# Kernel optimization log

Hardware: AMD Instinct MI355X
Metric: run time of the kernel (lower is better)

The kernel has to match this reference:

```python
import jax, jax.numpy as jnp
import numpy as np

EPS = 1e-5
K_NBR = 21   # num_neighbors + 1 (self)
PSI = 4


def _bn(x, g, b):
    # BatchNorm (training-mode forward): channel-last, normalize over all other axes
    axes = tuple(range(x.ndim - 1))
    m = jnp.mean(x, axis=axes, keepdims=True)
    v = jnp.var(x, axis=axes, keepdims=True)
    return (x - m) * jax.lax.rsqrt(v + EPS) * g + b


def setup_inputs() -> dict:
    key = jax.random.key(0)
    ks = jax.random.split(key, 16)
    B, N, Cin, Cout = 4, 2048, 64, 256
    h = Cout // 2
    w_ch = Cout // PSI
    heads = 2 * PSI - 1

    def w(k, o, i):
        return jax.random.normal(k, (o, i), dtype=jnp.float32) * (1.0 / np.sqrt(i))

    p = {}
    p['xyz'] = jax.random.normal(ks[0], (B, N, 3), dtype=jnp.float32)
    p['f'] = jax.random.normal(ks[1], (B, Cin, N), dtype=jnp.float32)
    p['W_geo'] = w(ks[2], h, 6);       p['g_geo'] = jnp.ones(h);   p['b_geo'] = jnp.zeros(h)
    p['W_feat'] = w(ks[3], h, 2 * Cin); p['g_feat'] = jnp.ones(h); p['b_feat'] = jnp.zeros(h)
    p['g_bn'] = jnp.ones(Cout); p['b_bn'] = jnp.zeros(Cout)
    p['W_q'] = w(ks[4], Cout, Cout); p['g_q'] = jnp.ones(Cout); p['b_q'] = jnp.zeros(Cout)
    p['W_k'] = w(ks[5], Cout, Cout); p['g_k'] = jnp.ones(Cout); p['b_k'] = jnp.zeros(Cout)
    p['W_v'] = w(ks[6], Cout, Cout); p['g_v'] = jnp.ones(Cout); p['b_v'] = jnp.zeros(Cout)
    p['W_fus'] = w(ks[7], Cout, heads * w_ch); p['bias_fus'] = jnp.zeros(Cout)
    p['g_fus'] = jnp.ones(Cout); p['b_fus'] = jnp.zeros(Cout)
    p['g_ln'] = jnp.ones(Cout); p['b_ln'] = jnp.zeros(Cout)
    p['W_mlp'] = w(ks[8], Cout, Cout); p['bias_mlp'] = jnp.zeros(Cout)
    return p


def reference(xyz, f, W_geo, g_geo, b_geo, W_feat, g_feat, b_feat, g_bn, b_bn,
              W_q, g_q, b_q, W_k, g_k, b_k, W_v, g_v, b_v,
              W_fus, bias_fus, g_fus, b_fus, g_ln, b_ln, W_mlp, bias_mlp):
    B, N, _ = xyz.shape
    Cout = g_bn.shape[0]
    w_ch = Cout // PSI
    d_sh = w_ch // 2
    heads = 2 * PSI - 1

    # ---- PositionFusion: KNN grouping ----
    sq = jnp.sum(xyz * xyz, axis=-1)                                   # [B,N]
    d2 = sq[:, :, None] + sq[:, None, :] - 2.0 * jnp.einsum('bnd,bmd->bnm', xyz, xyz)
    _, idx = jax.lax.top_k(-d2, K_NBR)                                 # [B,N,K]

    grouped_xyz = jax.vmap(lambda p, i: p[i])(xyz, idx)                # [B,N,K,3]
    xyz_diff = grouped_xyz - xyz[:, :, None, :]
    geo_in = jnp.concatenate(
        [jnp.broadcast_to(xyz[:, :, None, :], grouped_xyz.shape), xyz_diff], axis=-1)  # [B,N,K,6]

    ft = jnp.transpose(f, (0, 2, 1))                                   # [B,N,Cin]
    grouped_f = jax.vmap(lambda p, i: p[i])(ft, idx)                   # [B,N,K,Cin]
    feat_in = jnp.concatenate(
        [grouped_f, jnp.broadcast_to(ft[:, :, None, :], grouped_f.shape)], axis=-1)    # [B,N,K,2Cin]

    geo = jax.nn.relu(_bn(jnp.einsum('bnki,oi->bnko', geo_in, W_geo), g_geo, b_geo))
    fea = jax.nn.relu(_bn(jnp.einsum('bnki,oi->bnko', feat_in, W_feat), g_feat, b_feat))
    feature_ = jnp.max(jnp.concatenate([geo, fea], axis=-1), axis=2)   # [B,N,Cout] (maxpool over K)

    # ---- BatchNorm1d ----
    x = _bn(feature_, g_bn, b_bn)

    # ---- Shifted-channel multi-head attention ----
    q = jax.nn.relu(_bn(jnp.einsum('bnc,oc->bno', x, W_q), g_q, b_q))
    k = jax.nn.relu(_bn(jnp.einsum('bnc,oc->bno', x, W_k), g_k, b_k))
    v = jax.nn.relu(_bn(jnp.einsum('bnc,oc->bno', x, W_v), g_v, b_v))

    qh = jnp.stack([q[..., m * d_sh:m * d_sh + w_ch] for m in range(heads)], axis=1)  # [B,H,N,w]
    kh = jnp.stack([k[..., m * d_sh:m * d_sh + w_ch] for m in range(heads)], axis=1)
    vh = jnp.stack([v[..., m * d_sh:m * d_sh + w_ch] for m in range(heads)], axis=1)

    a = jax.nn.softmax(jnp.einsum('bhnc,bhmc->bhnm', qh, kh), axis=-1)  # [B,H,N,N]
    o = jnp.einsum('bhnm,bhmc->bhnc', a, vh)                            # [B,H,N,w]
    O = jnp.transpose(o, (0, 2, 1, 3)).reshape(B, N, heads * w_ch)      # channel-concat per head

    fus = jax.nn.relu(_bn(jnp.einsum('bnc,oc->bno', O, W_fus) + bias_fus, g_fus, b_fus))

    feature__ = fus + feature_                                          # residual

    # ---- LayerNorm over channels ----
    m = jnp.mean(feature__, axis=-1, keepdims=True)
    var = jnp.var(feature__, axis=-1, keepdims=True)
    y = (feature__ - m) * jax.lax.rsqrt(var + EPS) * g_ln + b_ln

    out = feature__ + (jnp.einsum('bnc,oc->bno', y, W_mlp) + bias_mlp)
    return jnp.transpose(out, (0, 2, 1))                                # [B,Cout,N] like torch
```

## Files before the change

kernel.cpp:

```cpp
#include <hip/hip_runtime.h>
#include <math.h>

#define NB    4
#define NPTS  2048
#define ROWS  (NB*NPTS)
#define CIN   64
#define COUT  256
#define KNBR  21
#define NHEADS 7
#define WCH   64
#define DSH   32

typedef __attribute__((ext_vector_type(8))) short short8;
typedef __attribute__((ext_vector_type(4))) float floatx4;

__device__ __forceinline__ ushort f2bf(float x) {
    unsigned u = __float_as_uint(x);
    u += 0x7fffu + ((u >> 16) & 1u);
    return (ushort)(u >> 16);
}

template<int N>
__device__ __forceinline__ float dpp_ror16(float x) {
    return __int_as_float(__builtin_amdgcn_update_dpp(
        0, __float_as_int(x), 0x120 | N, 0xF, 0xF, true));
}
__device__ __forceinline__ float dpp_max16(float x) {
    x = fmaxf(x, dpp_ror16<1>(x));
    x = fmaxf(x, dpp_ror16<2>(x));
    x = fmaxf(x, dpp_ror16<4>(x));
    x = fmaxf(x, dpp_ror16<8>(x));
    return x;
}
__device__ __forceinline__ float dpp_sum16(float x) {
    x += dpp_ror16<1>(x);
    x += dpp_ror16<2>(x);
    x += dpp_ror16<4>(x);
    x += dpp_ror16<8>(x);
    return x;
}

template<int CTRL, int RMASK>
__device__ __forceinline__ unsigned dpp_umin_step(unsigned x) {
    unsigned t = (unsigned)__builtin_amdgcn_update_dpp((int)x, (int)x, CTRL, RMASK, 0xF, false);
    return (t < x) ? t : x;
}
__device__ __forceinline__ unsigned wave_min_u32(unsigned x) {
    x = dpp_umin_step<0x111, 0xF>(x);
    x = dpp_umin_step<0x112, 0xF>(x);
    x = dpp_umin_step<0x114, 0xF>(x);
    x = dpp_umin_step<0x118, 0xF>(x);
    x = dpp_umin_step<0x142, 0xA>(x);
    x = dpp_umin_step<0x143, 0xC>(x);
    return (unsigned)__builtin_amdgcn_readlane((int)x, 63);
}

__global__ __launch_bounds__(256) void prep_knn(const float* __restrict__ f, const float* __restrict__ Wf,
                                                const float* __restrict__ xyz, const float* __restrict__ Wg,
                                                const float* __restrict__ W_q, const float* __restrict__ W_k,
                                                const float* __restrict__ W_v,
                                                float* __restrict__ X, float* __restrict__ A,
                                                ushort* __restrict__ Wb, float* __restrict__ sums,
                                                int* __restrict__ idx) {
    __shared__ float4 SXQ[2048];
    int t = threadIdx.x;
    int blk = blockIdx.x;
    if (blk < 512) {
        float* As = (float*)SXQ;
        float* Ws = As + 16*68;
        int bx = blk & 127, by = blk >> 7;
        if (by == 0 && bx < 12) sums[bx*256 + t] = 0.f;
        int gid = (by*128 + bx)*256 + t;
        for (int i = gid; i < 196608; i += 131072) {
            const float* Wsrc = (i < 65536) ? W_q : (i < 131072) ? W_k : W_v;
            Wb[i] = f2bf(Wsrc[i & 65535]);
        }
        int r0 = bx * 64, n0 = by * 64;
        for (int e = t; e < 4096; e += 256) {
            int row = r0 + (e >> 6), c = n0 + (e & 63), cc = c & 127;
            float x = xyz[row*3], y = xyz[row*3+1], z = xyz[row*3+2];
            const float* w = Wg + cc*6;
            float s = (c < 128) ? ((w[3]*x + w[4]*y) + w[5]*z)
                                : (((w[0]-w[3])*x + (w[1]-w[4])*y) + (w[2]-w[5])*z);
            A[(size_t)row*256 + c] = s;
        }
        int b = r0 >> 11, nbase = r0 & 2047;
        int tx = t & 15, ty = t >> 4;
        float acc[4][4];
#pragma unroll
        for (int i = 0; i < 4; i++)
#pragma unroll
            for (int j = 0; j < 4; j++) acc[i][j] = 0.f;
        int m64 = t & 63, kg = t >> 6;
        int lk = t & 15, lm = t >> 4;
        for (int k0 = 0; k0 < 64; k0 += 16) {
#pragma unroll
            for (int p = 0; p < 4; p++) {
                int k = kg*4 + p;
                As[k*68 + m64] = f[(size_t)b*CIN*NPTS + (size_t)(k0 + k)*NPTS + nbase + m64];
            }
#pragma unroll
            for (int i2 = 0; i2 < 4; i2++) {
                int cg = n0 + lm + 16*i2;
                Ws[lk*68 + lm + 16*i2] = Wf[(size_t)(cg & 127)*128 + (cg >> 7)*64 + k0 + lk];
            }
            __syncthreads();
#pragma unroll
            for (int kq = 0; kq < 16; kq++) {
                float4 a  = *(const float4*)&As[kq*68 + 4*ty];
                float4 b4 = *(const float4*)&Ws[kq*68 + 4*tx];
                float av[4] = {a.x, a.y, a.z, a.w};
                float bv[4] = {b4.x, b4.y, b4.z, b4.w};
#pragma unroll
                for (int i = 0; i < 4; i++)
#pragma unroll
                    for (int j = 0; j < 4; j++) acc[i][j] = fmaf(av[i], bv[j], acc[i][j]);
            }
            __syncthreads();
        }
#pragma unroll
        for (int i = 0; i < 4; i++)
#pragma unroll
            for (int j = 0; j < 4; j++)
                X[(size_t)(r0 + 4*ty + i)*256 + n0 + 4*tx + j] = acc[i][j];
        return;
    }
    int kb = blk - 512;
    int b = kb >> 9;
    int g = kb & 511;
    for (int m = t; m < NPTS; m += 256) {
        float x = xyz[(size_t)b*NPTS*3 + m*3];
        float y = xyz[(size_t)b*NPTS*3 + m*3 + 1];
        float z = xyz[(size_t)b*NPTS*3 + m*3 + 2];
        SXQ[m] = make_float4(x, y, z, (x*x + y*y) + z*z);
    }
    __syncthreads();
    int w = t >> 6, lane = t & 63;
    int n = g*4 + w;
    float4 q4 = SXQ[n];
    float qx = q4.x, qy = q4.y, qz = q4.z, sqn = q4.w;
    unsigned key[32];
#pragma unroll
    for (int i = 0; i < 32; i++) {
        int m = lane + (i << 6);
        float4 p = SXQ[m];
        float dt = (qx*p.x + qy*p.y) + qz*p.z;
        float d2 = fmaxf((sqn + p.w) - 2.0f*dt, 0.f);
        key[i] = (__float_as_uint(d2) & 0xFFFFF800u) | (unsigned)m;
    }
    unsigned winkey = 0xFFFFFFFFu;
    for (int kk = 0; kk < 32; kk++) {
        unsigned lv = key[0];
#pragma unroll
        for (int i = 1; i < 32; i++) lv = (key[i] < lv) ? key[i] : lv;
        unsigned win = wave_min_u32(lv);
        if (lane == kk) winkey = win;
        unsigned widx = win & 2047u;
        int slot = (int)(widx >> 6);
        bool own = (lane == (int)(widx & 63u));
#pragma unroll
        for (int i = 0; i < 32; i++)
            if (i == slot && own) key[i] = 0xFFFFFFFFu;
    }
    double d2r;
    int mr;
    {
        double qx64 = (double)qx, qy64 = (double)qy, qz64 = (double)qz;
        double sqn64 = qx64*qx64 + qy64*qy64 + qz64*qz64;
        if (lane < 32) {
            mr = (int)(winkey & 2047u);
            float4 p = SXQ[mr];
            double x = (double)p.x, y = (double)p.y, z = (double)p.z;
            double sqm = x*x + y*y + z*z;
            double dt  = qx64*x + qy64*y + qz64*z;
            d2r = (sqn64 + sqm) - 2.0*dt;
        } else {
            d2r = INFINITY; mr = 0x7FFFFFFF;
        }
    }
#pragma unroll
    for (int k = 2; k <= 32; k <<= 1) {
#pragma unroll
        for (int j = k >> 1; j > 0; j >>= 1) {
            double od = __shfl_xor(d2r, j, 64);
            int    om = __shfl_xor(mr, j, 64);
            bool up    = ((lane & k) == 0);
            bool lower = ((lane & j) == 0);
            bool oless = (od < d2r) || (od == d2r && om < mr);
            bool keepOther = up ? (lower ? oless : !oless) : (lower ? !oless : oless);
            if (keepOther) { d2r = od; mr = om; }
        }
    }
    if (lane < KNBR)
        idx[((size_t)b*NPTS + n)*KNBR + lane] = mr;
}

__global__ __launch_bounds__(256) void stats_gf(const float* __restrict__ geoBC, const float* __restrict__ featAC,
                                                const int* __restrict__ idx, const float* __restrict__ g_geo,
                                                const float* __restrict__ g_feat,
                                                float* __restrict__ sums, float* __restrict__ xsel) {
    int c = threadIdx.x;
    int cc = c & 127;
    const float* base = (c < 128) ? geoBC : featAC;
    bool wantmax = ((c < 128) ? g_geo[cc] : g_feat[cc]) >= 0.f;
    float s = 0.f, ss = 0.f;
    int r0 = blockIdx.x * 32;
    for (int r = r0; r < r0 + 32; r++) {
        int b = r >> 11;
        float ctr = base[(size_t)r*256 + 128 + cc];
        float mx = -1e30f, mn = 1e30f;
        const int* ip = idx + (size_t)r*KNBR;
        for (int kk = 0; kk < KNBR; kk++) {
            int j = ip[kk];
            float xv = ctr + base[((size_t)(b*NPTS + j))*256 + cc];
            mx = fmaxf(mx, xv); mn = fminf(mn, xv);
            s += xv; ss += xv*xv;
        }
        xsel[(size_t)r*256 + c] = wantmax ? mx : mn;
    }
    atomicAdd(&sums[c], s);
    atomicAdd(&sums[256 + c], ss);
}

__global__ __launch_bounds__(256) void feature_maxsel(const float* __restrict__ xsel, const float* __restrict__ sums,
                                                      const float* __restrict__ g_geo, const float* __restrict__ b_geo,
                                                      const float* __restrict__ g_feat, const float* __restrict__ b_feat,
                                                      float* __restrict__ feat, float* __restrict__ sums_bn1) {
    int c = threadIdx.x;
    const float inv = 1.0f / (float)(ROWS*KNBR);
    float mean = sums[c]*inv;
    float var  = sums[256+c]*inv - mean*mean;
    float g  = (c < 128) ? g_geo[c] : g_feat[c-128];
    float bb = (c < 128) ? b_geo[c] : b_feat[c-128];
    float sc = g / sqrtf(var + 1e-5f);
    float tt = bb - mean*sc;
    float s = 0.f, ss = 0.f;
    int r0 = blockIdx.x*32;
    for (int r = r0; r < r0+32; r++) {
        size_t i = (size_t)r*256 + c;
        float y = fmaxf(fmaf(sc, xsel[i], tt), 0.f);
        feat[i] = y; s += y; ss += y*y;
    }
    atomicAdd(&sums_bn1[c], s); atomicAdd(&sums_bn1[256+c], ss);
}

__global__ __launch_bounds__(256) void gemm_qkv(const float* __restrict__ Af, const float* __restrict__ sums_in,
                                                const float* __restrict__ g_bn, const float* __restrict__ b_bn,
                                                const ushort* __restrict__ Wb,
                                                float* __restrict__ QKVF, float* __restrict__ sums) {
    __shared__ float bns[2][256];
    __shared__ float red[4][256][2];
    int t = threadIdx.x;
    int r0 = blockIdx.x * 64, g = blockIdx.y;
    int w = t >> 6, lane = t & 63;
    int r15 = lane & 15, quad = lane >> 4;
    {
        float mean = sums_in[512 + t] * (1.0f/(float)ROWS);
        float var  = sums_in[768 + t] * (1.0f/(float)ROWS) - mean*mean;
        float sc = g_bn[t] / sqrtf(var + 1e-5f);
        bns[0][t] = sc;
        bns[1][t] = b_bn[t] - mean*sc;
    }
    __syncthreads();
    short8 aq[8];
    {
        const float* ap = Af + (size_t)(r0 + 16*w + r15)*256;
#pragma unroll
        for (int kc = 0; kc < 8; kc++) {
            int k0 = 32*kc + 8*quad;
            float4 a0 = *(const float4*)&ap[k0];
            float4 a1 = *(const float4*)&ap[k0+4];
            float4 s0 = *(const float4*)&bns[0][k0];
            float4 s1 = *(const float4*)&bns[0][k0+4];
            float4 h0 = *(const float4*)&bns[1][k0];
            float4 h1 = *(const float4*)&bns[1][k0+4];
            ushort u8[8];
            u8[0] = f2bf(fmaf(s0.x, a0.x, h0.x)); u8[1] = f2bf(fmaf(s0.y, a0.y, h0.y));
            u8[2] = f2bf(fmaf(s0.z, a0.z, h0.z)); u8[3] = f2bf(fmaf(s0.w, a0.w, h0.w));
            u8[4] = f2bf(fmaf(s1.x, a1.x, h1.x)); u8[5] = f2bf(fmaf(s1.y, a1.y, h1.y));
            u8[6] = f2bf(fmaf(s1.z, a1.z, h1.z)); u8[7] = f2bf(fmaf(s1.w, a1.w, h1.w));
            aq[kc] = *(short8*)u8;
        }
    }
    floatx4 zero4 = {0.f, 0.f, 0.f, 0.f};
    floatx4 acc[16];
#pragma unroll
    for (int st = 0; st < 16; st++) acc[st] = zero4;
    const ushort* wbase = Wb + (size_t)g*65536 + (size_t)r15*256 + 8*quad;
#pragma unroll
    for (int st = 0; st < 16; st++) {
        const ushort* wp = wbase + (size_t)(16*st)*256;
#pragma unroll
        for (int kc = 0; kc < 8; kc++) {
            short8 bf = *(const short8*)(wp + 32*kc);
            acc[st] = __builtin_amdgcn_mfma_f32_16x16x32_bf16(aq[kc], bf, acc[st], 0, 0, 0);
        }
    }
#pragma unroll
    for (int st = 0; st < 16; st++) {
        float s  = (acc[st][0] + acc[st][1]) + (acc[st][2] + acc[st][3]);
        float q2 = (acc[st][0]*acc[st][0] + acc[st][1]*acc[st][1]) +
                   (acc[st][2]*acc[st][2] + acc[st][3]*acc[st][3]);
        s  += __shfl_xor(s, 16, 64);  s  += __shfl_xor(s, 32, 64);
        q2 += __shfl_xor(q2, 16, 64); q2 += __shfl_xor(q2, 32, 64);
        if (lane < 16) { red[w][16*st + r15][0] = s; red[w][16*st + r15][1] = q2; }
#pragma unroll
        for (int reg = 0; reg < 4; reg++)
            QKVF[(size_t)(r0 + 16*w + 4*quad + reg)*768 + g*256 + 16*st + r15] = acc[st][reg];
    }
    __syncthreads();
    {
        float s = red[0][t][0] + red[1][t][0] + red[2][t][0] + red[3][t][0];
        float q = red[0][t][1] + red[1][t][1] + red[2][t][1] + red[3][t][1];
        atomicAdd(&sums[1024 + g*512 + t], s);
        atomicAdd(&sums[1024 + g*512 + 256 + t], q);
    }
}

__global__ __launch_bounds__(256) void affine_qkv(const float* __restrict__ QKVF, const float* __restrict__ sums,
                                                  const float* __restrict__ g_q, const float* __restrict__ b_q,
                                                  const float* __restrict__ g_k, const float* __restrict__ b_k,
                                                  const float* __restrict__ g_v, const float* __restrict__ b_v,
                                                  ushort* __restrict__ qk, ushort* __restrict__ vt) {
    __shared__ float sts[6][256];
    __shared__ ushort tile[64][72];
    int t = threadIdx.x;
    {
        const float* gs[3] = {g_q, g_k, g_v};
        const float* bs[3] = {b_q, b_k, b_v};
#pragma unroll
        for (int g = 0; g < 3; g++) {
            float mean = sums[1024 + g*512 + t] * (1.0f/(float)ROWS);
            float var  = sums[1024 + g*512 + 256 + t] * (1.0f/(float)ROWS) - mean*mean;
            float sc = gs[g][t] / sqrtf(var + 1e-5f);
            sts[2*g][t] = sc;
            sts[2*g+1][t] = bs[g][t] - mean*sc;
        }
    }
    __syncthreads();
    int r0 = blockIdx.x * 64, c0 = blockIdx.y * 64;
    int b = r0 >> 11, nbase = r0 & 2047;
    if (c0 < 512) {
#pragma unroll
        for (int rep = 0; rep < 16; rep++) {
            int e = t + 256*rep;
            int row = e >> 6, c = e & 63;
            int col = c0 + c, g = col >> 8, cc = col & 255;
            float v = QKVF[(size_t)(r0 + row)*768 + col];
            v = fmaxf(fmaf(sts[2*g][cc], v, sts[2*g+1][cc]), 0.f);
            qk[(size_t)(r0 + row)*512 + col] = f2bf(v);
        }
    } else {
#pragma unroll
        for (int rep = 0; rep < 16; rep++) {
            int e = t + 256*rep;
            int row = e >> 6, c = e & 63;
            int col = c0 + c, cc = col & 255;
            float v = QKVF[(size_t)(r0 + row)*768 + col];
            v = fmaxf(fmaf(sts[4][cc], v, sts[5][cc]), 0.f);
            tile[c][row] = f2bf(v);
        }
        __syncthreads();
#pragma unroll
        for (int rep = 0; rep < 16; rep++) {
            int e = t + 256*rep;
            int cc = e >> 6, nn = e & 63;
            vt[((size_t)(b*256 + (c0 - 512) + cc))*2048 + nbase + nn] = tile[cc][nn];
        }
    }
}

__global__ __launch_bounds__(256) void attn2(const ushort* __restrict__ qk, const ushort* __restrict__ vt,
                                             float* __restrict__ obuf) {
    __shared__ ushort Ksh[64*72];
    __shared__ ushort Vts[64*72];
    __shared__ ushort Psh[128*72];
    int h = blockIdx.y, b = blockIdx.z;
    int r0 = blockIdx.x * 128;
    int t = threadIdx.x;
    int w = t >> 6, lane = t & 63;
    int r15 = lane & 15, quad = lane >> 4;
    size_t rowbase = (size_t)b*NPTS;
    int hoff = h*DSH;

    short8 aq[2][2];
#pragma unroll
    for (int u = 0; u < 2; u++)
#pragma unroll
        for (int s = 0; s < 2; s++)
            aq[u][s] = *(const short8*)(qk + (rowbase + r0 + 64*u + 16*w + r15)*512 + hoff + 32*s + 8*quad);

    floatx4 zero4 = {0.f, 0.f, 0.f, 0.f};
    floatx4 oacc[2][4];
    float mrun[2][4], lrun[2][4];
#pragma unroll
    for (int u = 0; u < 2; u++)
#pragma unroll
        for (int i = 0; i < 4; i++) { oacc[u][i] = zero4; mrun[u][i] = -1e30f; lrun[u][i] = 0.f; }

    for (int m0 = 0; m0 < NPTS; m0 += 64) {
#pragma unroll
        for (int rep = 0; rep < 2; rep++) {
            int e = t + 256*rep;
            int rr = e >> 3, c = e & 7;
            *(uint4*)&Ksh[rr*72 + 8*c] =
                *(const uint4*)(qk + (rowbase + m0 + rr)*512 + 256 + hoff + 8*c);
            *(uint4*)&Vts[rr*72 + 8*c] =
                *(const uint4*)(vt + ((size_t)(b*256 + hoff + rr))*2048 + m0 + 8*c);
        }
        __syncthreads();

        floatx4 sacc[2][4];
#pragma unroll
        for (int u = 0; u < 2; u++)
#pragma unroll
            for (int tt = 0; tt < 4; tt++) sacc[u][tt] = zero4;
#pragma unroll
        for (int tt = 0; tt < 4; tt++) {
            int key = 16*tt + r15;
#pragma unroll
            for (int s = 0; s < 2; s++) {
                short8 kf = *(const short8*)&Ksh[key*72 + 32*s + 8*quad];
#pragma unroll
                for (int u = 0; u < 2; u++)
                    sacc[u][tt] = __builtin_amdgcn_mfma_f32_16x16x32_bf16(aq[u][s], kf, sacc[u][tt], 0, 0, 0);
            }
        }

        float pm[2][4][4];
#pragma unroll
        for (int u = 0; u < 2; u++)
#pragma unroll
            for (int reg = 0; reg < 4; reg++) {
                float rmax = fmaxf(fmaxf(sacc[u][0][reg], sacc[u][1][reg]),
                                   fmaxf(sacc[u][2][reg], sacc[u][3][reg]));
                rmax = dpp_max16(rmax);
                float mnew = fmaxf(mrun[u][reg], rmax);
                float alpha = __expf(mrun[u][reg] - mnew);
                float rs = 0.f;
#pragma unroll
                for (int tt = 0; tt < 4; tt++) {
                    float p = __expf(sacc[u][tt][reg] - mnew);
                    pm[u][tt][reg] = p; rs += p;
                }
                rs = dpp_sum16(rs);
                lrun[u][reg] = lrun[u][reg]*alpha + rs;
                mrun[u][reg] = mnew;
#pragma unroll
                for (int td = 0; td < 4; td++) oacc[u][td][reg] *= alpha;
            }

#pragma unroll
        for (int u = 0; u < 2; u++)
#pragma unroll
            for (int reg = 0; reg < 4; reg++) {
                int row = 64*u + 16*w + 4*quad + reg;
#pragma unroll
                for (int tt = 0; tt < 4; tt++)
                    Psh[row*72 + 16*tt + r15] = f2bf(pm[u][tt][reg]);
            }
        __syncthreads();

#pragma unroll
        for (int s = 0; s < 2; s++) {
            short8 pf[2];
#pragma unroll
            for (int u = 0; u < 2; u++)
                pf[u] = *(const short8*)&Psh[(64*u + 16*w + r15)*72 + 32*s + 8*quad];
#pragma unroll
            for (int td = 0; td < 4; td++) {
                short8 vf = *(const short8*)&Vts[(16*td + r15)*72 + 32*s + 8*quad];
#pragma unroll
                for (int u = 0; u < 2; u++)
                    oacc[u][td] = __builtin_amdgcn_mfma_f32_16x16x32_bf16(pf[u], vf, oacc[u][td], 0, 0, 0);
            }
        }
        __syncthreads();
    }

#pragma unroll
    for (int u = 0; u < 2; u++)
#pragma unroll
        for (int reg = 0; reg < 4; reg++) {
            int grow = r0 + 64*u + 16*w + 4*quad + reg;
            float invl = 1.f / lrun[u][reg];
#pragma unroll
            for (int td = 0; td < 4; td++)
                obuf[(rowbase + grow)*(size_t)(NHEADS*WCH) + h*WCH + 16*td + r15] = oacc[u][td][reg]*invl;
        }
}

__global__ __launch_bounds__(256) void gemm_fus(const float* __restrict__ A, const float* __restrict__ W,
                                                const float* __restrict__ bias, float* __restrict__ C,
                                                float* __restrict__ sums) {
    __shared__ float As[16][68];
    __shared__ float Ws[16][68];
    __shared__ float red[4][64][2];
    int t = threadIdx.x;
    int tx = t & 15, ty = t >> 4;
    int r0 = blockIdx.x * 64, n0 = blockIdx.y * 64;
    float acc[4][4];
#pragma unroll
    for (int i = 0; i < 4; i++)
#pragma unroll
        for (int j = 0; j < 4; j++) acc[i][j] = 0.f;
    int lk = t & 15, lm = t >> 4;
    for (int k0 = 0; k0 < 448; k0 += 16) {
#pragma unroll
        for (int i2 = 0; i2 < 4; i2++) {
            As[lk][lm + 16*i2] = A[(size_t)(r0 + lm + 16*i2)*448 + k0 + lk];
            Ws[lk][lm + 16*i2] = W[(size_t)(n0 + lm + 16*i2)*448 + k0 + lk];
        }
        __syncthreads();
#pragma unroll
        for (int kq = 0; kq < 16; kq++) {
            float4 a  = *(const float4*)&As[kq][4*ty];
            float4 b4 = *(const float4*)&Ws[kq][4*tx];
            float av[4] = {a.x, a.y, a.z, a.w};
            float bv[4] = {b4.x, b4.y, b4.z, b4.w};
#pragma unroll
            for (int i = 0; i < 4; i++)
#pragma unroll
                for (int j = 0; j < 4; j++) acc[i][j] = fmaf(av[i], bv[j], acc[i][j]);
        }
        __syncthreads();
    }
    float ps[4], pss[4];
#pragma unroll
    for (int j = 0; j < 4; j++) { ps[j] = 0.f; pss[j] = 0.f; }
#pragma unroll
    for (int i = 0; i < 4; i++)
#pragma unroll
        for (int j = 0; j < 4; j++) {
            float v = acc[i][j] + bias[n0 + 4*tx + j];
            C[(size_t)(r0 + 4*ty + i)*256 + n0 + 4*tx + j] = v;
            ps[j] += v; pss[j] += v*v;
        }
#pragma unroll
    for (int j = 0; j < 4; j++) {
        ps[j]  += __shfl_xor(ps[j], 16, 64);  ps[j]  += __shfl_xor(ps[j], 32, 64);
        pss[j] += __shfl_xor(pss[j], 16, 64); pss[j] += __shfl_xor(pss[j], 32, 64);
    }
    int wv = t >> 6, lane = t & 63;
    if (lane < 16) {
#pragma unroll
        for (int j = 0; j < 4; j++) {
            red[wv][4*tx + j][0] = ps[j];
            red[wv][4*tx + j][1] = pss[j];
        }
    }
    __syncthreads();
    if (t < 128) {
        int col = t >> 1, which = t & 1;
        float v = red[0][col][which] + red[1][col][which] + red[2][col][which] + red[3][col][which];
        atomicAdd(&sums[2560 + which*256 + n0 + col], v);
    }
}

__global__ __launch_bounds__(256) void ln_fused(float* __restrict__ fusp, const float* __restrict__ feature,
                                                const float* __restrict__ sums,
                                                const float* __restrict__ g_fus, const float* __restrict__ b_fus,
                                                const float* __restrict__ g_ln, const float* __restrict__ b_ln,
                                                float* __restrict__ y) {
    int r = blockIdx.x, c = threadIdx.x;
    float mean0 = sums[2560 + c] * (1.0f/(float)ROWS);
    float var0  = sums[2560 + 256 + c] * (1.0f/(float)ROWS) - mean0*mean0;
    float scF = g_fus[c] / sqrtf(var0 + 1e-5f);
    float shF = b_fus[c] - mean0*scF;
    size_t i = (size_t)r*256 + c;
    float fus = fmaxf(fmaf(scF, fusp[i], shF), 0.f);
    float v = fus + feature[i];
    float s = v, ss = v*v;
    for (int m = 1; m < 64; m <<= 1) { s += __shfl_xor(s, m, 64); ss += __shfl_xor(ss, m, 64); }
    __shared__ float red[8];
    int wave = c >> 6, lane = c & 63;
    if (lane == 0) { red[wave] = s; red[4+wave] = ss; }
    __syncthreads();
    s  = red[0]+red[1]+red[2]+red[3];
    ss = red[4]+red[5]+red[6]+red[7];
    float mean = s * (1.f/256.f);
    float var  = ss * (1.f/256.f) - mean*mean;
    float rin  = 1.f/sqrtf(var + 1e-5f);
    fusp[i] = v;
    y[i] = (v - mean)*rin*g_ln[c] + b_ln[c];
}

__global__ __launch_bounds__(256) void gemm_mlp(const float* __restrict__ A, const float* __restrict__ W,
                                                const float* __restrict__ bias, const float* __restrict__ FF,
                                                float* __restrict__ outp) {
    __shared__ float As[16][68];
    __shared__ float Ws[16][68];
    __shared__ float tr[64][65];
    int t = threadIdx.x;
    int tx = t & 15, ty = t >> 4;
    int r0 = blockIdx.x * 64, n0 = blockIdx.y * 64;
    float acc[4][4];
#pragma unroll
    for (int i = 0; i < 4; i++)
#pragma unroll
        for (int j = 0; j < 4; j++) acc[i][j] = 0.f;
    int lk = t & 15, lm = t >> 4;
    for (int k0 = 0; k0 < 256; k0 += 16) {
#pragma unroll
        for (int i2 = 0; i2 < 4; i2++) {
            As[lk][lm + 16*i2] = A[(size_t)(r0 + lm + 16*i2)*256 + k0 + lk];
            Ws[lk][lm + 16*i2] = W[(size_t)(n0 + lm + 16*i2)*256 + k0 + lk];
        }
        __syncthreads();
#pragma unroll
        for (int kq = 0; kq < 16; kq++) {
            float4 a  = *(const float4*)&As[kq][4*ty];
            float4 b4 = *(const float4*)&Ws[kq][4*tx];
            float av[4] = {a.x, a.y, a.z, a.w};
            float bv[4] = {b4.x, b4.y, b4.z, b4.w};
#pragma unroll
            for (int i = 0; i < 4; i++)
#pragma unroll
                for (int j = 0; j < 4; j++) acc[i][j] = fmaf(av[i], bv[j], acc[i][j]);
        }
        __syncthreads();
    }
#pragma unroll
    for (int i = 0; i < 4; i++)
#pragma unroll
        for (int j = 0; j < 4; j++) {
            float v = acc[i][j] + bias[n0 + 4*tx + j] + FF[(size_t)(r0 + 4*ty + i)*256 + n0 + 4*tx + j];
            tr[4*tx + j][4*ty + i] = v;
        }
    __syncthreads();
    int b = r0 >> 11, nbase = r0 & 2047;
#pragma unroll
    for (int rep = 0; rep < 16; rep++) {
        int e = t + 256*rep;
        int cl = e >> 6, nl = e & 63;
        outp[((size_t)(b*256 + n0 + cl))*2048 + nbase + nl] = tr[cl][nl];
    }
}

extern "C" void kernel_launch(void* const* d_in, const int* in_sizes, int n_in,
                              void* d_out, int out_size, void* d_ws, size_t ws_size,
                              hipStream_t stream) {
    const float* xyz    = (const float*)d_in[0];
    const float* f      = (const float*)d_in[1];
    const float* W_geo  = (const float*)d_in[2];
    const float* g_geo  = (const float*)d_in[3];
    const float* b_geo  = (const float*)d_in[4];
    const float* W_feat = (const float*)d_in[5];
    const float* g_feat = (const float*)d_in[6];
    const float* b_feat = (const float*)d_in[7];
    const float* g_bn   = (const float*)d_in[8];
    const float* b_bn   = (const float*)d_in[9];
    const float* W_q    = (const float*)d_in[10];
    const float* g_q    = (const float*)d_in[11];
    const float* b_q    = (const float*)d_in[12];
    const float* W_k    = (const float*)d_in[13];
    const float* g_k    = (const float*)d_in[14];
    const float* b_k    = (const float*)d_in[15];
    const float* W_v    = (const float*)d_in[16];
    const float* g_v    = (const float*)d_in[17];
    const float* b_v    = (const float*)d_in[18];
    const float* W_fus  = (const float*)d_in[19];
    const float* bias_fus = (const float*)d_in[20];
    const float* g_fus  = (const float*)d_in[21];
    const float* b_fus  = (const float*)d_in[22];
    const float* g_ln   = (const float*)d_in[23];
    const float* b_ln   = (const float*)d_in[24];
    const float* W_mlp  = (const float*)d_in[25];
    const float* bias_mlp = (const float*)d_in[26];

    float* ws = (float*)d_ws;
    const size_t MBF = 262144;
    float* SUMS  = ws;
    int*   IDX   = (int*)(ws + 16384);
    float* A     = ws + 1*MBF;
    float* X     = ws + 9*MBF;
    ushort* QK16 = (ushort*)(ws + 9*MBF);
    float* YB    = ws + 9*MBF;
    float* CSEL  = ws + 17*MBF;
    float* QKVF  = ws + 17*MBF;
    float* OBUF  = ws + 17*MBF;
    float* FUSP  = ws + 31*MBF;
    ushort* VT16 = (ushort*)(ws + 41*MBF);
    ushort* WB16 = (ushort*)(ws + 45*MBF);

    prep_knn<<<2560, 256, 0, stream>>>(f, W_feat, xyz, W_geo, W_q, W_k, W_v,
                                       X, A, WB16, SUMS, IDX);
    stats_gf<<<256, 256, 0, stream>>>(A, X, IDX, g_geo, g_feat, SUMS, CSEL);
    feature_maxsel<<<256, 256, 0, stream>>>(CSEL, SUMS, g_geo, b_geo, g_feat, b_feat, A, SUMS + 512);
    gemm_qkv<<<dim3(128, 3), 256, 0, stream>>>(A, SUMS, g_bn, b_bn, WB16, QKVF, SUMS);
    affine_qkv<<<dim3(128, 12), 256, 0, stream>>>(QKVF, SUMS, g_q, b_q, g_k, b_k, g_v, b_v, QK16, VT16);
    attn2<<<dim3(NPTS/128, NHEADS, NB), 256, 0, stream>>>(QK16, VT16, OBUF);
    gemm_fus<<<dim3(128, 4), 256, 0, stream>>>(OBUF, W_fus, bias_fus, FUSP, SUMS);
    ln_fused<<<ROWS, 256, 0, stream>>>(FUSP, A, SUMS, g_fus, b_fus, g_ln, b_ln, YB);
    gemm_mlp<<<dim3(128, 4), 256, 0, stream>>>(YB, W_mlp, bias_mlp, FUSP, (float*)d_out);
}
```

Measured before the change: 435.6 us.

## Split attention over keys, merge in MFMA fusion GEMM, fuse LayerNorm into MLP

Attention is split into two halves over the key dimension, doubling the grid, and each half writes unnormalised partial outputs plus running max and sum. The fusion GEMM merges the two partials with log-sum-exp weights and now runs on bf16 MFMA using a W_fus copy converted in the prep kernel. The LayerNorm kernel is folded into the MLP GEMM, which recomputes the per-row normalisation. The log2(e) scale is folded into the q affine transform so the softmax can use exp2. Together these raise attention occupancy and remove a kernel launch and a full intermediate write/read, at the cost of extra partial-output traffic, bf16 rounding in the fusion GEMM, and each MLP block recomputing the LayerNorm over all 256 channels.

```diff
diff --git a/kernel.cpp b/kernel.cpp
--- a/kernel.cpp
+++ b/kernel.cpp
@@ -10,6 +10,7 @@
 #define NHEADS 7
 #define WCH   64
 #define DSH   32
+#define LOG2E 1.4426950408889634f
 
 typedef __attribute__((ext_vector_type(8))) short short8;
 typedef __attribute__((ext_vector_type(4))) float floatx4;
@@ -58,7 +59,7 @@
 __global__ __launch_bounds__(256) void prep_knn(const float* __restrict__ f, const float* __restrict__ Wf,
                                                 const float* __restrict__ xyz, const float* __restrict__ Wg,
                                                 const float* __restrict__ W_q, const float* __restrict__ W_k,
-                                                const float* __restrict__ W_v,
+                                                const float* __restrict__ W_v, const float* __restrict__ W_fus,
                                                 float* __restrict__ X, float* __restrict__ A,
                                                 ushort* __restrict__ Wb, float* __restrict__ sums,
                                                 int* __restrict__ idx) {
@@ -71,9 +72,13 @@
         int bx = blk & 127, by = blk >> 7;
         if (by == 0 && bx < 12) sums[bx*256 + t] = 0.f;
         int gid = (by*128 + bx)*256 + t;
-        for (int i = gid; i < 196608; i += 131072) {
-            const float* Wsrc = (i < 65536) ? W_q : (i < 131072) ? W_k : W_v;
-            Wb[i] = f2bf(Wsrc[i & 65535]);
+        for (int i = gid; i < 311296; i += 131072) {
+            const float* Wsrc; int off;
+            if (i < 65536)       { Wsrc = W_q;   off = i; }
+            else if (i < 131072) { Wsrc = W_k;   off = i - 65536; }
+            else if (i < 196608) { Wsrc = W_v;   off = i - 131072; }
+            else                 { Wsrc = W_fus; off = i - 196608; }
+            Wb[i] = f2bf(Wsrc[off]);
         }
         int r0 = bx * 64, n0 = by * 64;
         for (int e = t; e < 4096; e += 256) {
@@ -333,8 +338,10 @@
             float mean = sums[1024 + g*512 + t] * (1.0f/(float)ROWS);
             float var  = sums[1024 + g*512 + 256 + t] * (1.0f/(float)ROWS) - mean*mean;
             float sc = gs[g][t] / sqrtf(var + 1e-5f);
+            float sh = bs[g][t] - mean*sc;
+            if (g == 0) { sc *= LOG2E; sh *= LOG2E; }
             sts[2*g][t] = sc;
-            sts[2*g+1][t] = bs[g][t] - mean*sc;
+            sts[2*g+1][t] = sh;
         }
     }
     __syncthreads();
@@ -370,18 +377,21 @@
     }
 }
 
-__global__ __launch_bounds__(256) void attn2(const ushort* __restrict__ qk, const ushort* __restrict__ vt,
-                                             float* __restrict__ obuf) {
+__global__ __launch_bounds__(256) void attn_split(const ushort* __restrict__ qk, const ushort* __restrict__ vt,
+                                                  float* __restrict__ OP0, float* __restrict__ OP1,
+                                                  float2* __restrict__ ML) {
     __shared__ ushort Ksh[64*72];
     __shared__ ushort Vts[64*72];
     __shared__ ushort Psh[128*72];
-    int h = blockIdx.y, b = blockIdx.z;
+    int h = blockIdx.y;
+    int z = blockIdx.z; int b = z >> 1, ks = z & 1;
     int r0 = blockIdx.x * 128;
     int t = threadIdx.x;
     int w = t >> 6, lane = t & 63;
     int r15 = lane & 15, quad = lane >> 4;
     size_t rowbase = (size_t)b*NPTS;
     int hoff = h*DSH;
+    float* OP = ks ? OP1 : OP0;
 
     short8 aq[2][2];
 #pragma unroll
@@ -398,7 +408,8 @@
 #pragma unroll
         for (int i = 0; i < 4; i++) { oacc[u][i] = zero4; mrun[u][i] = -1e30f; lrun[u][i] = 0.f; }
 
-    for (int m0 = 0; m0 < NPTS; m0 += 64) {
+    int mstart = ks << 10;
+    for (int m0 = mstart; m0 < mstart + 1024; m0 += 64) {
 #pragma unroll
         for (int rep = 0; rep < 2; rep++) {
             int e = t + 256*rep;
@@ -436,11 +447,11 @@
                                    fmaxf(sacc[u][2][reg], sacc[u][3][reg]));
                 rmax = dpp_max16(rmax);
                 float mnew = fmaxf(mrun[u][reg], rmax);
-                float alpha = __expf(mrun[u][reg] - mnew);
+                float alpha = exp2f(mrun[u][reg] - mnew);
                 float rs = 0.f;
 #pragma unroll
                 for (int tt = 0; tt < 4; tt++) {
-                    float p = __expf(sacc[u][tt][reg] - mnew);
+                    float p = exp2f(sacc[u][tt][reg] - mnew);
                     pm[u][tt][reg] = p; rs += p;
                 }
                 rs = dpp_sum16(rs);
@@ -483,38 +494,168 @@
 #pragma unroll
         for (int reg = 0; reg < 4; reg++) {
             int grow = r0 + 64*u + 16*w + 4*quad + reg;
-            float invl = 1.f / lrun[u][reg];
 #pragma unroll
             for (int td = 0; td < 4; td++)
-                obuf[(rowbase + grow)*(size_t)(NHEADS*WCH) + h*WCH + 16*td + r15] = oacc[u][td][reg]*invl;
-        }
-}
-
-__global__ __launch_bounds__(256) void gemm_fus(const float* __restrict__ A, const float* __restrict__ W,
+                OP[(rowbase + grow)*(size_t)(NHEADS*WCH) + h*WCH + 16*td + r15] = oacc[u][td][reg];
+            if (r15 == 0)
+                ML[((size_t)ks*ROWS + rowbase + grow)*NHEADS + h] = make_float2(mrun[u][reg], lrun[u][reg]);
+        }
+}
+
+__global__ __launch_bounds__(256) void gemm_fus(const float* __restrict__ OP0, const float* __restrict__ OP1,
+                                                const float2* __restrict__ ML, const ushort* __restrict__ Wb,
                                                 const float* __restrict__ bias, float* __restrict__ C,
                                                 float* __restrict__ sums) {
-    __shared__ float As[16][68];
+    __shared__ float W2s[64][8][2];
+    __shared__ float red[4][128][2];
+    int t = threadIdx.x;
+    int r0 = blockIdx.x * 64, n0 = blockIdx.y * 128;
+    int w = t >> 6, lane = t & 63;
+    int r15 = lane & 15, quad = lane >> 4;
+    for (int e = t; e < 448; e += 256) {
+        int row = e / 7, h = e % 7;
+        float2 a  = ML[(size_t)(r0 + row)*NHEADS + h];
+        float2 c2 = ML[((size_t)ROWS + r0 + row)*NHEADS + h];
+        float mm = fmaxf(a.x, c2.x);
+        float e0 = exp2f(a.x - mm), e1 = exp2f(c2.x - mm);
+        float inv = 1.f / (a.y*e0 + c2.y*e1);
+        W2s[row][h][0] = e0*inv;
+        W2s[row][h][1] = e1*inv;
+    }
+    __syncthreads();
+    int arow = 16*w + r15;
+    short8 aq[14];
+    {
+        const float* p0 = OP0 + (size_t)(r0 + arow)*448;
+        const float* p1 = OP1 + (size_t)(r0 + arow)*448;
+#pragma unroll
+        for (int kc = 0; kc < 14; kc++) {
+            int k0 = 32*kc + 8*quad;
+            int h = k0 >> 6;
+            float w0 = W2s[arow][h][0], w1 = W2s[arow][h][1];
+            float4 x0 = *(const float4*)&p0[k0];
+            float4 x1 = *(const float4*)&p1[k0];
+            float4 y0 = *(const float4*)&p0[k0+4];
+            float4 y1 = *(const float4*)&p1[k0+4];
+            ushort u8[8];
+            u8[0] = f2bf(x0.x*w0 + x1.x*w1); u8[1] = f2bf(x0.y*w0 + x1.y*w1);
+            u8[2] = f2bf(x0.z*w0 + x1.z*w1); u8[3] = f2bf(x0.w*w0 + x1.w*w1);
+            u8[4] = f2bf(y0.x*w0 + y1.x*w1); u8[5] = f2bf(y0.y*w0 + y1.y*w1);
+            u8[6] = f2bf(y0.z*w0 + y1.z*w1); u8[7] = f2bf(y0.w*w0 + y1.w*w1);
+            aq[kc] = *(short8*)u8;
+        }
+    }
+    floatx4 zero4 = {0.f, 0.f, 0.f, 0.f};
+    floatx4 acc[8];
+#pragma unroll
+    for (int st = 0; st < 8; st++) acc[st] = zero4;
+    const ushort* wbase = Wb + 196608 + (size_t)(n0 + r15)*448 + 8*quad;
+#pragma unroll
+    for (int st = 0; st < 8; st++) {
+        const ushort* wp = wbase + (size_t)(16*st)*448;
+#pragma unroll
+        for (int kc = 0; kc < 14; kc++) {
+            short8 bf = *(const short8*)(wp + 32*kc);
+            acc[st] = __builtin_amdgcn_mfma_f32_16x16x32_bf16(aq[kc], bf, acc[st], 0, 0, 0);
+        }
+    }
+#pragma unroll
+    for (int st = 0; st < 8; st++) {
+        int col = n0 + 16*st + r15;
+        float bi = bias[col];
+        float v0 = acc[st][0] + bi, v1 = acc[st][1] + bi, v2 = acc[st][2] + bi, v3 = acc[st][3] + bi;
+        float s  = (v0 + v1) + (v2 + v3);
+        float q2 = (v0*v0 + v1*v1) + (v2*v2 + v3*v3);
+        s  += __shfl_xor(s, 16, 64);  s  += __shfl_xor(s, 32, 64);
+        q2 += __shfl_xor(q2, 16, 64); q2 += __shfl_xor(q2, 32, 64);
+        if (lane < 16) { red[w][16*st + r15][0] = s; red[w][16*st + r15][1] = q2; }
+        C[(size_t)(r0 + 16*w + 4*quad + 0)*256 + col] = v0;
+        C[(size_t)(r0 + 16*w + 4*quad + 1)*256 + col] = v1;
+        C[(size_t)(r0 + 16*w + 4*quad + 2)*256 + col] = v2;
+        C[(size_t)(r0 + 16*w + 4*quad + 3)*256 + col] = v3;
+    }
+    __syncthreads();
+    {
+        int col = t >> 1, which = t & 1;
+        float v = red[0][col][which] + red[1][col][which] + red[2][col][which] + red[3][col][which];
+        atomicAdd(&sums[2560 + which*256 + n0 + col], v);
+    }
+}
+
+__global__ __launch_bounds__(256) void gemm_mlp_ln(const float* __restrict__ FUSP, const float* __restrict__ A,
+                                                   const float* __restrict__ sums,
+                                                   const float* __restrict__ g_fus, const float* __restrict__ b_fus,
+                                                   const float* __restrict__ g_ln, const float* __restrict__ b_ln,
+                                                   const float* __restrict__ W, const float* __restrict__ bias,
+                                                   float* __restrict__ outp) {
+    __shared__ float Ys[256][68];
+    __shared__ float FFs[64][65];
     __shared__ float Ws[16][68];
-    __shared__ float red[4][64][2];
+    __shared__ float tr[64][65];
+    __shared__ float SC[256], SH[256], GL[256], BL[256];
     int t = threadIdx.x;
+    int r0 = blockIdx.x*64, n0 = blockIdx.y*64;
+    {
+        float mean0 = sums[2560 + t] * (1.0f/(float)ROWS);
+        float var0  = sums[2560 + 256 + t] * (1.0f/(float)ROWS) - mean0*mean0;
+        float sc = g_fus[t] / sqrtf(var0 + 1e-5f);
+        SC[t] = sc; SH[t] = b_fus[t] - mean0*sc;
+        GL[t] = g_ln[t]; BL[t] = b_ln[t];
+    }
+    __syncthreads();
+    int row = t >> 2, seg = t & 3;
+    size_t rb = (size_t)(r0 + row)*256;
+    float4 vv[16];
+    float s = 0.f, ss = 0.f;
+#pragma unroll
+    for (int j = 0; j < 16; j++) {
+        int c = seg*64 + 4*j;
+        float4 fp = *(const float4*)&FUSP[rb + c];
+        float4 fe = *(const float4*)&A[rb + c];
+        float4 sc4 = *(const float4*)&SC[c];
+        float4 sh4 = *(const float4*)&SH[c];
+        float4 v;
+        v.x = fmaxf(fmaf(sc4.x, fp.x, sh4.x), 0.f) + fe.x;
+        v.y = fmaxf(fmaf(sc4.y, fp.y, sh4.y), 0.f) + fe.y;
+        v.z = fmaxf(fmaf(sc4.z, fp.z, sh4.z), 0.f) + fe.z;
+        v.w = fmaxf(fmaf(sc4.w, fp.w, sh4.w), 0.f) + fe.w;
+        vv[j] = v;
+        s  += (v.x + v.y) + (v.z + v.w);
+        ss += (v.x*v.x + v.y*v.y) + (v.z*v.z + v.w*v.w);
+        if (seg == blockIdx.y) *(float4*)&FFs[row][4*j] = v;
+    }
+    s  += __shfl_xor(s, 1, 64);  s  += __shfl_xor(s, 2, 64);
+    ss += __shfl_xor(ss, 1, 64); ss += __shfl_xor(ss, 2, 64);
+    float mean = s * (1.f/256.f);
+    float var  = ss * (1.f/256.f) - mean*mean;
+    float rin  = 1.f/sqrtf(var + 1e-5f);
+#pragma unroll
+    for (int j = 0; j < 16; j++) {
+        int c = seg*64 + 4*j;
+        float4 gl = *(const float4*)&GL[c];
+        float4 bl = *(const float4*)&BL[c];
+        float4 v = vv[j];
+        Ys[c+0][row] = (v.x - mean)*rin*gl.x + bl.x;
+        Ys[c+1][row] = (v.y - mean)*rin*gl.y + bl.y;
+        Ys[c+2][row] = (v.z - mean)*rin*gl.z + bl.z;
+        Ys[c+3][row] = (v.w - mean)*rin*gl.w + bl.w;
+    }
+    __syncthreads();
     int tx = t & 15, ty = t >> 4;
-    int r0 = blockIdx.x * 64, n0 = blockIdx.y * 64;
+    int lk = t & 15, lm = t >> 4;
     float acc[4][4];
 #pragma unroll
     for (int i = 0; i < 4; i++)
 #pragma unroll
         for (int j = 0; j < 4; j++) acc[i][j] = 0.f;
-    int lk = t & 15, lm = t >> 4;
-    for (int k0 = 0; k0 < 448; k0 += 16) {
-#pragma unroll
-        for (int i2 = 0; i2 < 4; i2++) {
-            As[lk][lm + 16*i2] = A[(size_t)(r0 + lm + 16*i2)*448 + k0 + lk];
-            Ws[lk][lm + 16*i2] = W[(size_t)(n0 + lm + 16*i2)*448 + k0 + lk];
-        }
+    for (int k0 = 0; k0 < 256; k0 += 16) {
+#pragma unroll
+        for (int i2 = 0; i2 < 4; i2++)
+            Ws[lk][lm + 16*i2] = W[(size_t)(n0 + lm + 16*i2)*256 + k0 + lk];
         __syncthreads();
 #pragma unroll
         for (int kq = 0; kq < 16; kq++) {
-            float4 a  = *(const float4*)&As[kq][4*ty];
+            float4 a  = *(const float4*)&Ys[k0 + kq][4*ty];
             float4 b4 = *(const float4*)&Ws[kq][4*tx];
             float av[4] = {a.x, a.y, a.z, a.w};
             float bv[4] = {b4.x, b4.y, b4.z, b4.w};
@@ -525,106 +666,11 @@
         }
         __syncthreads();
     }
-    float ps[4], pss[4];
-#pragma unroll
-    for (int j = 0; j < 4; j++) { ps[j] = 0.f; pss[j] = 0.f; }
 #pragma unroll
     for (int i = 0; i < 4; i++)
 #pragma unroll
         for (int j = 0; j < 4; j++) {
-            float v = acc[i][j] + bias[n0 + 4*tx + j];
-            C[(size_t)(r0 + 4*ty + i)*256 + n0 + 4*tx + j] = v;
-            ps[j] += v; pss[j] += v*v;
-        }
-#pragma unroll
-    for (int j = 0; j < 4; j++) {
-        ps[j]  += __shfl_xor(ps[j], 16, 64);  ps[j]  += __shfl_xor(ps[j], 32, 64);
-        pss[j] += __shfl_xor(pss[j], 16, 64); pss[j] += __shfl_xor(pss[j], 32, 64);
-    }
-    int wv = t >> 6, lane = t & 63;
-    if (lane < 16) {
-#pragma unroll
-        for (int j = 0; j < 4; j++) {
-            red[wv][4*tx + j][0] = ps[j];
-            red[wv][4*tx + j][1] = pss[j];
-        }
-    }
-    __syncthreads();
-    if (t < 128) {
-        int col = t >> 1, which = t & 1;
-        float v = red[0][col][which] + red[1][col][which] + red[2][col][which] + red[3][col][which];
-        atomicAdd(&sums[2560 + which*256 + n0 + col], v);
-    }
-}
-
-__global__ __launch_bounds__(256) void ln_fused(float* __restrict__ fusp, const float* __restrict__ feature,
-                                                const float* __restrict__ sums,
-                                                const float* __restrict__ g_fus, const float* __restrict__ b_fus,
-                                                const float* __restrict__ g_ln, const float* __restrict__ b_ln,
-                                                float* __restrict__ y) {
-    int r = blockIdx.x, c = threadIdx.x;
-    float mean0 = sums[2560 + c] * (1.0f/(float)ROWS);
-    float var0  = sums[2560 + 256 + c] * (1.0f/(float)ROWS) - mean0*mean0;
-    float scF = g_fus[c] / sqrtf(var0 + 1e-5f);
-    float shF = b_fus[c] - mean0*scF;
-    size_t i = (size_t)r*256 + c;
-    float fus = fmaxf(fmaf(scF, fusp[i], shF), 0.f);
-    float v = fus + feature[i];
-    float s = v, ss = v*v;
-    for (int m = 1; m < 64; m <<= 1) { s += __shfl_xor(s, m, 64); ss += __shfl_xor(ss, m, 64); }
-    __shared__ float red[8];
-    int wave = c >> 6, lane = c & 63;
-    if (lane == 0) { red[wave] = s; red[4+wave] = ss; }
-    __syncthreads();
-    s  = red[0]+red[1]+red[2]+red[3];
-    ss = red[4]+red[5]+red[6]+red[7];
-    float mean = s * (1.f/256.f);
-    float var  = ss * (1.f/256.f) - mean*mean;
-    float rin  = 1.f/sqrtf(var + 1e-5f);
-    fusp[i] = v;
-    y[i] = (v - mean)*rin*g_ln[c] + b_ln[c];
-}
-
-__global__ __launch_bounds__(256) void gemm_mlp(const float* __restrict__ A, const float* __restrict__ W,
-                                                const float* __restrict__ bias, const float* __restrict__ FF,
-                                                float* __restrict__ outp) {
-    __shared__ float As[16][68];
-    __shared__ float Ws[16][68];
-    __shared__ float tr[64][65];
-    int t = threadIdx.x;
-    int tx = t & 15, ty = t >> 4;
-    int r0 = blockIdx.x * 64, n0 = blockIdx.y * 64;
-    float acc[4][4];
-#pragma unroll
-    for (int i = 0; i < 4; i++)
-#pragma unroll
-        for (int j = 0; j < 4; j++) acc[i][j] = 0.f;
-    int lk = t & 15, lm = t >> 4;
-    for (int k0 = 0; k0 < 256; k0 += 16) {
-#pragma unroll
-        for (int i2 = 0; i2 < 4; i2++) {
-            As[lk][lm + 16*i2] = A[(size_t)(r0 + lm + 16*i2)*256 + k0 + lk];
-            Ws[lk][lm + 16*i2] = W[(size_t)(n0 + lm + 16*i2)*256 + k0 + lk];
-        }
-        __syncthreads();
-#pragma unroll
-        for (int kq = 0; kq < 16; kq++) {
-            float4 a  = *(const float4*)&As[kq][4*ty];
-            float4 b4 = *(const float4*)&Ws[kq][4*tx];
-            float av[4] = {a.x, a.y, a.z, a.w};
-            float bv[4] = {b4.x, b4.y, b4.z, b4.w};
-#pragma unroll
-            for (int i = 0; i < 4; i++)
-#pragma unroll
-                for (int j = 0; j < 4; j++) acc[i][j] = fmaf(av[i], bv[j], acc[i][j]);
-        }
-        __syncthreads();
-    }
-#pragma unroll
-    for (int i = 0; i < 4; i++)
-#pragma unroll
-        for (int j = 0; j < 4; j++) {
-            float v = acc[i][j] + bias[n0 + 4*tx + j] + FF[(size_t)(r0 + 4*ty + i)*256 + n0 + 4*tx + j];
+            float v = acc[i][j] + bias[n0 + 4*tx + j] + FFs[4*ty + i][4*tx + j];
             tr[4*tx + j][4*ty + i] = v;
         }
     __syncthreads();
@@ -675,22 +721,23 @@
     float* A     = ws + 1*MBF;
     float* X     = ws + 9*MBF;
     ushort* QK16 = (ushort*)(ws + 9*MBF);
-    float* YB    = ws + 9*MBF;
+    float* FUSP  = ws + 9*MBF;
     float* CSEL  = ws + 17*MBF;
     float* QKVF  = ws + 17*MBF;
-    float* OBUF  = ws + 17*MBF;
-    float* FUSP  = ws + 31*MBF;
-    ushort* VT16 = (ushort*)(ws + 41*MBF);
-    ushort* WB16 = (ushort*)(ws + 45*MBF);
-
-    prep_knn<<<2560, 256, 0, stream>>>(f, W_feat, xyz, W_geo, W_q, W_k, W_v,
+    float* OP0   = ws + 17*MBF;
+    float* OP1   = ws + 31*MBF;
+    ushort* VT16 = (ushort*)(ws + 45*MBF);
+    ushort* WB16 = (ushort*)(ws + 49*MBF);
+    float2* ML   = (float2*)(ws + 49*MBF + 163840);
+
+    prep_knn<<<2560, 256, 0, stream>>>(f, W_feat, xyz, W_geo, W_q, W_k, W_v, W_fus,
                                        X, A, WB16, SUMS, IDX);
     stats_gf<<<256, 256, 0, stream>>>(A, X, IDX, g_geo, g_feat, SUMS, CSEL);
     feature_maxsel<<<256, 256, 0, stream>>>(CSEL, SUMS, g_geo, b_geo, g_feat, b_feat, A, SUMS + 512);
     gemm_qkv<<<dim3(128, 3), 256, 0, stream>>>(A, SUMS, g_bn, b_bn, WB16, QKVF, SUMS);
     affine_qkv<<<dim3(128, 12), 256, 0, stream>>>(QKVF, SUMS, g_q, b_q, g_k, b_k, g_v, b_v, QK16, VT16);
-    attn2<<<dim3(NPTS/128, NHEADS, NB), 256, 0, stream>>>(QK16, VT16, OBUF);
-    gemm_fus<<<dim3(128, 4), 256, 0, stream>>>(OBUF, W_fus, bias_fus, FUSP, SUMS);
-    ln_fused<<<ROWS, 256, 0, stream>>>(FUSP, A, SUMS, g_fus, b_fus, g_ln, b_ln, YB);
-    gemm_mlp<<<dim3(128, 4), 256, 0, stream>>>(YB, W_mlp, bias_mlp, FUSP, (float*)d_out);
-}
+    attn_split<<<dim3(NPTS/128, NHEADS, NB*2), 256, 0, stream>>>(QK16, VT16, OP0, OP1, ML);
+    gemm_fus<<<dim3(128, 2), 256, 0, stream>>>(OP0, OP1, ML, WB16, bias_fus, FUSP, SUMS);
+    gemm_mlp_ln<<<dim3(128, 4), 256, 0, stream>>>(FUSP, A, SUMS, g_fus, b_fus, g_ln, b_ln,
+                                                  W_mlp, bias_mlp, (float*)d_out);
+}
```

Measured after the change: 452.3 us. +3.9%, slower.
